# Optimization experiments

Measured on AMD Instinct MI355X. Metric: run time of the kernel, lower is better.

The kernel has to match this reference:

```python
import jax, jax.numpy as jnp
import numpy as np

B, T, I = 4096, 256, 8
H1, H2 = 100, 50


def _init(key, shape, fan):
    # PyTorch LSTM/Linear default: U(-1/sqrt(fan), 1/sqrt(fan))
    bound = 1.0 / np.sqrt(fan)
    return jax.random.uniform(key, shape, jnp.float32, -bound, bound)


def setup_inputs() -> dict:
    key = jax.random.key(0)
    ks = jax.random.split(key, 12)
    x = jax.random.normal(ks[0], (B, T, I), jnp.float32)
    return {
        "x": x,
        "W_ih1": _init(ks[1], (4 * H1, I), H1),
        "W_hh1": _init(ks[2], (4 * H1, H1), H1),
        "b_ih1": _init(ks[3], (4 * H1,), H1),
        "b_hh1": _init(ks[4], (4 * H1,), H1),
        "W_ih2": _init(ks[5], (4 * H2, H1), H2),
        "W_hh2": _init(ks[6], (4 * H2, H2), H2),
        "b_ih2": _init(ks[7], (4 * H2,), H2),
        "b_hh2": _init(ks[8], (4 * H2,), H2),
        "Wd": _init(ks[9], (1, H2), H2),
        "bd": _init(ks[10], (1,), H2),
    }


def _lstm_layer(x, W_ih, W_hh, b_ih, b_hh, H, return_seq):
    # x: [B, T, F]. PyTorch gate order: i, f, g, o. Zero initial state.
    Bn = x.shape[0]
    xg = jnp.einsum("btf,gf->btg", x, W_ih) + b_ih + b_hh  # [B, T, 4H]

    def step(carry, xg_t):
        h, c = carry
        g = xg_t + h @ W_hh.T  # [B, 4H]
        i, f, gg, o = jnp.split(g, 4, axis=-1)
        c = jax.nn.sigmoid(f) * c + jax.nn.sigmoid(i) * jnp.tanh(gg)
        h = jax.nn.sigmoid(o) * jnp.tanh(c)
        return (h, c), (h if return_seq else 0.0)

    init = (jnp.zeros((Bn, H), x.dtype), jnp.zeros((Bn, H), x.dtype))
    (h_last, _), hs = jax.lax.scan(step, init, jnp.swapaxes(xg, 0, 1))
    if return_seq:
        return jnp.swapaxes(hs, 0, 1)  # [B, T, H]
    return h_last  # [B, H]


def reference(x, W_ih1, W_hh1, b_ih1, b_hh1, W_ih2, W_hh2, b_ih2, b_hh2, Wd, bd):
    out1 = _lstm_layer(x, W_ih1, W_hh1, b_ih1, b_hh1, H1, return_seq=True)
    h2 = _lstm_layer(out1, W_ih2, W_hh2, b_ih2, b_hh2, H2, return_seq=False)
    # dropout(p=0.2) is identity in eval mode
    return h2 @ Wd.T + bd  # [B, 1]
```

## Files before the change

### kernel.cpp

```cpp
#include <hip/hip_runtime.h>
#include <math.h>

#define TT 256
#define H1 100
#define H2 50
#define NT 512
#define NBLK 256
#define ROWS 16

typedef __attribute__((ext_vector_type(8))) short bf16x8;
typedef __attribute__((ext_vector_type(4))) float f32x4;

__device__ __forceinline__ float sigf(float x) {
    return __builtin_amdgcn_rcpf(1.0f + __expf(-x));
}
__device__ __forceinline__ float tanhfast(float x) {
    return 1.0f - 2.0f * __builtin_amdgcn_rcpf(1.0f + __expf(2.0f * x));
}
__device__ __forceinline__ short f2bf(float f) {
    union { float f; unsigned u; } v; v.f = f;
    unsigned r = v.u + 0x7FFFu + ((v.u >> 16) & 1u);
    return (short)(r >> 16);
}

__device__ __forceinline__ int off_frag(int K, int R) {
    return (K >> 5) * 1024 + ((K >> 3) & 3) * 256 + R * 16 + (K & 7) * 2;
}

#define MFMA(w, b, c) __builtin_amdgcn_mfma_f32_16x16x32_bf16(w, b, c, 0, 0, 0)

__device__ __forceinline__ float cellup(const f32x4& a, float& cst) {
    const float is = sigf(a[0]), fs = sigf(a[1]);
    const float gt = tanhfast(a[2]), os = sigf(a[3]);
    const float c = fs * cst + is * gt;
    cst = c;
    return os * tanhfast(c);
}

__device__ __forceinline__ void load_w1(bf16x8* dst, int T, int r, int q,
                                        const float* W_hh1, const float* W_ih1) {
    const int jp = T * 16 + r, g = jp & 3, uu = jp >> 2;
#pragma unroll
    for (int c = 0; c < 4; ++c) {
        bf16x8 w;
#pragma unroll
        for (int i = 0; i < 8; ++i) {
            const int k = c * 32 + q * 8 + i;
            float f = 0.f;
            if (k < H1) f = W_hh1[(g * H1 + uu) * H1 + k];
            else if (k < H1 + 8) f = W_ih1[(g * H1 + uu) * 8 + (k - H1)];
            w[i] = f2bf(f);
        }
        dst[c] = w;
    }
}
__device__ __forceinline__ void load_w2(bf16x8* dst, int t2, int r, int q,
                                        const float* W_ih2, const float* W_hh2) {
    const int jp = t2 * 16 + r, g = jp & 3, uu = jp >> 2;
    const bool ok = uu < H2;
#pragma unroll
    for (int c = 0; c < 6; ++c) {
        bf16x8 w;
#pragma unroll
        for (int i = 0; i < 8; ++i) {
            float f = 0.f;
            if (ok) {
                if (c < 4) {
                    const int k = c * 32 + q * 8 + i;
                    if (k < H1) f = W_ih2[(g * H2 + uu) * H1 + k];
                } else {
                    const int k2 = (c - 4) * 32 + q * 8 + i;
                    if (k2 < H2) f = W_hh2[(g * H2 + uu) * H2 + k2];
                }
            }
            w[i] = f2bf(f);
        }
        dst[c] = w;
    }
}

__global__ __launch_bounds__(NT, 2) void lstm_ws3(
    const float* __restrict__ x,
    const float* __restrict__ W_ih1, const float* __restrict__ W_hh1,
    const float* __restrict__ b_ih1, const float* __restrict__ b_hh1,
    const float* __restrict__ W_ih2, const float* __restrict__ W_hh2,
    const float* __restrict__ b_ih2, const float* __restrict__ b_hh2,
    const float* __restrict__ Wd, const float* __restrict__ bd,
    float* __restrict__ out)
{
    __shared__ __align__(16) short xb[TT * ROWS * 8];
    __shared__ __align__(16) short A1h[2 * 4 * 64 * 8];
    __shared__ __align__(16) short h2b[2 * 2 * 64 * 8];
    __shared__ float hscr[ROWS * 52];

    const int tid = threadIdx.x;
    const int lane = tid & 63;
    const int wv = tid >> 6;
    const int r = lane & 15;
    const int q = lane >> 4;
    const int row0 = blockIdx.x * ROWS;

    char* const a1b = (char*)A1h;
    char* const h2bb = (char*)h2b;

    {
        const float* xg = x + (size_t)row0 * (TT * 8);
        for (int it = 0; it < 16; ++it) {
            const int f = (it * NT + tid) * 4;
            const float4 v = *(const float4*)(xg + f);
            const int rr = f >> 11, rem = f & 2047, t = rem >> 3, k = rem & 7;
            uint2 pk;
            pk.x = (unsigned short)f2bf(v.x) | ((unsigned)(unsigned short)f2bf(v.y) << 16);
            pk.y = (unsigned short)f2bf(v.z) | ((unsigned)(unsigned short)f2bf(v.w) << 16);
            *(uint2*)((char*)xb + t * 256 + rr * 16 + k * 2) = pk;
        }
    }
    for (int i = tid; i < 2 * 4 * 64 * 8; i += NT) A1h[i] = 0;
    for (int i = tid; i < 2 * 2 * 64 * 8; i += NT) h2b[i] = 0;

    bf16x8 wfA0[4], wfA1[4], wfA2[4], wfB[6], wfC[6];
    f32x4 bv0, bv1, bv2, bv3 = {0.f, 0.f, 0.f, 0.f}, bv4;
    int wof0, wof1, wof2, wof3 = 0, wof4;
    int hso3 = 0, hso4;
    bool ok3 = false;

    load_w1(wfA0, wv + 0, r, q, W_hh1, W_ih1);
    load_w1(wfA1, wv + 8, r, q, W_hh1, W_ih1);
    load_w1(wfA2, wv + 16, r, q, W_hh1, W_ih1);
    {
        const int u0 = (wv + 0) * 4 + q, u1 = (wv + 8) * 4 + q, u2_ = (wv + 16) * 4 + q;
#pragma unroll
        for (int g = 0; g < 4; ++g) {
            bv0[g] = b_ih1[g * H1 + u0] + b_hh1[g * H1 + u0];
            bv1[g] = b_ih1[g * H1 + u1] + b_hh1[g * H1 + u1];
            bv2[g] = b_ih1[g * H1 + u2_] + b_hh1[g * H1 + u2_];
        }
        wof0 = off_frag(u0, r); wof1 = off_frag(u1, r); wof2 = off_frag(u2_, r);
    }
    if (wv == 0) {
        load_w1(wfB, 24, r, q, W_hh1, W_ih1);
        wfB[4] = (bf16x8){0,0,0,0,0,0,0,0};
        wfB[5] = (bf16x8){0,0,0,0,0,0,0,0};
        const int u = 96 + q;
#pragma unroll
        for (int g = 0; g < 4; ++g) bv3[g] = b_ih1[g * H1 + u] + b_hh1[g * H1 + u];
        wof3 = off_frag(u, r);
        ok3 = true;
    } else if (wv <= 5) {
        load_w2(wfB, wv + 7, r, q, W_ih2, W_hh2);
        const int u2 = (wv + 7) * 4 + q;
        ok3 = (u2 < H2);
#pragma unroll
        for (int g = 0; g < 4; ++g)
            bv3[g] = ok3 ? (b_ih2[g * H2 + u2] + b_hh2[g * H2 + u2]) : 0.f;
        wof3 = off_frag(u2 & 63, r);
        hso3 = r * 52 + u2;
    } else {
#pragma unroll
        for (int c = 0; c < 6; ++c) wfB[c] = (bf16x8){0,0,0,0,0,0,0,0};
    }
    {
        load_w2(wfC, wv, r, q, W_ih2, W_hh2);
        const int u2 = wv * 4 + q;
#pragma unroll
        for (int g = 0; g < 4; ++g) bv4[g] = b_ih2[g * H2 + u2] + b_hh2[g * H2 + u2];
        wof4 = off_frag(u2, r);
        hso4 = r * 52 + u2;
    }

    float cst0 = 0.f, cst1 = 0.f, cst2 = 0.f, cst3 = 0.f, cst4 = 0.f;

    const bool wstage = ((tid >> 4) == 28);
    const int st = tid & 15;

    __syncthreads();
    if (tid < ROWS) {
        bf16x8 v = *(const bf16x8*)((const char*)xb + tid * 16);
        uint2 lo = ((const uint2*)&v)[0], hi = ((const uint2*)&v)[1];
        char* dst = a1b + 3 * 1024 + tid * 16;
        *(uint2*)(dst + 8) = lo;
        *(uint2*)(dst + 256) = hi;
    }
    __syncthreads();

    for (int s = 0; s < TT; ++s) {
        const int cur = s & 1;
        char* a1r = a1b + (cur << 12);
        char* h2r = h2bb + (cur << 11);
        char* a1w = a1b + ((cur ^ 1) << 12);
        char* h2w = h2bb + ((cur ^ 1) << 11);

        const bf16x8 bA0 = *(const bf16x8*)(a1r + 0 * 1024 + lane * 16);
        const bf16x8 bA1 = *(const bf16x8*)(a1r + 1 * 1024 + lane * 16);
        const bf16x8 bA2 = *(const bf16x8*)(a1r + 2 * 1024 + lane * 16);
        const bf16x8 bA3 = *(const bf16x8*)(a1r + 3 * 1024 + lane * 16);
        const bf16x8 bH0 = *(const bf16x8*)(h2r + 0 * 1024 + lane * 16);
        const bf16x8 bH1 = *(const bf16x8*)(h2r + 1 * 1024 + lane * 16);

        if (wstage && s + 1 < TT) {
            bf16x8 v = *(const bf16x8*)((const char*)xb + (s + 1) * 256 + st * 16);
            uint2 lo = ((const uint2*)&v)[0], hi = ((const uint2*)&v)[1];
            char* dst = a1w + 3 * 1024 + st * 16;
            *(uint2*)(dst + 8) = lo;
            *(uint2*)(dst + 256) = hi;
        }

        f32x4 a0 = MFMA(wfA0[0], bA0, bv0);
        f32x4 a1 = MFMA(wfA1[0], bA0, bv1);
        f32x4 a2 = MFMA(wfA2[0], bA0, bv2);
        f32x4 a3 = MFMA(wfB[0], bA0, bv3);
        f32x4 a4 = MFMA(wfC[0], bA0, bv4);
        a0 = MFMA(wfA0[1], bA1, a0);
        a1 = MFMA(wfA1[1], bA1, a1);
        a2 = MFMA(wfA2[1], bA1, a2);
        a3 = MFMA(wfB[1], bA1, a3);
        a4 = MFMA(wfC[1], bA1, a4);
        a0 = MFMA(wfA0[2], bA2, a0);
        a1 = MFMA(wfA1[2], bA2, a1);
        a2 = MFMA(wfA2[2], bA2, a2);
        a3 = MFMA(wfB[2], bA2, a3);
        a4 = MFMA(wfC[2], bA2, a4);
        a0 = MFMA(wfA0[3], bA3, a0);
        a1 = MFMA(wfA1[3], bA3, a1);
        a2 = MFMA(wfA2[3], bA3, a2);
        a3 = MFMA(wfB[3], bA3, a3);
        a4 = MFMA(wfC[3], bA3, a4);
        a3 = MFMA(wfB[4], bH0, a3);
        a4 = MFMA(wfC[4], bH0, a4);
        a3 = MFMA(wfB[5], bH1, a3);
        a4 = MFMA(wfC[5], bH1, a4);

        const float h0 = cellup(a0, cst0);
        const float h1v = cellup(a1, cst1);
        const float h2v = cellup(a2, cst2);
        *(short*)(a1w + wof0) = f2bf(h0);
        *(short*)(a1w + wof1) = f2bf(h1v);
        *(short*)(a1w + wof2) = f2bf(h2v);

        if (s > 0) {
            const float h4v = cellup(a4, cst4);
            *(short*)(h2w + wof4) = f2bf(h4v);
        }
        if (wv == 0 || (s > 0 && wv <= 5)) {
            const float h3v = cellup(a3, cst3);
            char* d3 = (wv == 0) ? a1w : h2w;
            if (ok3) *(short*)(d3 + wof3) = f2bf(h3v);
        }
        __syncthreads();
    }

    {
        char* a1r = a1b;
        char* h2r = h2bb;
        const bf16x8 bA0 = *(const bf16x8*)(a1r + 0 * 1024 + lane * 16);
        const bf16x8 bA1 = *(const bf16x8*)(a1r + 1 * 1024 + lane * 16);
        const bf16x8 bA2 = *(const bf16x8*)(a1r + 2 * 1024 + lane * 16);
        const bf16x8 bA3 = *(const bf16x8*)(a1r + 3 * 1024 + lane * 16);
        const bf16x8 bH0 = *(const bf16x8*)(h2r + 0 * 1024 + lane * 16);
        const bf16x8 bH1 = *(const bf16x8*)(h2r + 1 * 1024 + lane * 16);

        f32x4 a3 = MFMA(wfB[0], bA0, bv3);
        f32x4 a4 = MFMA(wfC[0], bA0, bv4);
        a3 = MFMA(wfB[1], bA1, a3);
        a4 = MFMA(wfC[1], bA1, a4);
        a3 = MFMA(wfB[2], bA2, a3);
        a4 = MFMA(wfC[2], bA2, a4);
        a3 = MFMA(wfB[3], bA3, a3);
        a4 = MFMA(wfC[3], bA3, a4);
        a3 = MFMA(wfB[4], bH0, a3);
        a4 = MFMA(wfC[4], bH0, a4);
        a3 = MFMA(wfB[5], bH1, a3);
        a4 = MFMA(wfC[5], bH1, a4);

        if (wv >= 1 && wv <= 5) {
            const float h3v = cellup(a3, cst3);
            if (ok3) hscr[hso3] = h3v;
        }
        {
            const float h4v = cellup(a4, cst4);
            hscr[hso4] = h4v;
        }
        __syncthreads();
    }

    if (tid < ROWS) {
        float acc = bd[0];
#pragma unroll 2
        for (int u = 0; u < H2; ++u) acc = fmaf(hscr[tid * 52 + u], Wd[u], acc);
        out[row0 + tid] = acc;
    }
}

extern "C" void kernel_launch(void* const* d_in, const int* in_sizes, int n_in,
                              void* d_out, int out_size, void* d_ws, size_t ws_size,
                              hipStream_t stream) {
    const float* x     = (const float*)d_in[0];
    const float* W_ih1 = (const float*)d_in[1];
    const float* W_hh1 = (const float*)d_in[2];
    const float* b_ih1 = (const float*)d_in[3];
    const float* b_hh1 = (const float*)d_in[4];
    const float* W_ih2 = (const float*)d_in[5];
    const float* W_hh2 = (const float*)d_in[6];
    const float* b_ih2 = (const float*)d_in[7];
    const float* b_hh2 = (const float*)d_in[8];
    const float* Wd    = (const float*)d_in[9];
    const float* bd    = (const float*)d_in[10];
    float* out = (float*)d_out;

    hipLaunchKernelGGL(lstm_ws3, dim3(NBLK), dim3(NT), 0, stream,
                       x, W_ih1, W_hh1, b_ih1, b_hh1,
                       W_ih2, W_hh2, b_ih2, b_hh2, Wd, bd, out);
}
```

Baseline: 380.0 us.

## Double waves per block to spread LSTM gate tiles across 16 wavefronts

The block grows from 8 to 16 wavefronts, and each wave now owns at most three gate tiles instead of five. The 25 layer-1 tiles and 13 layer-2 tiles are reassigned: waves 0-8 take two layer-1 tiles, waves 9-15 take one layer-1 and one layer-2 tile, and waves 0-5 take an extra layer-2 tile. The aim is to shorten the serial MFMA and cell-update chain per wave on every timestep. In exchange, each barrier now synchronises more waves, and occupancy drops from 2 blocks per CU to 1 with a 1024-thread block.

Result: faster. 367.8 us (-3.2%).

```diff
diff --git a/kernel.cpp b/kernel.cpp
--- a/kernel.cpp
+++ b/kernel.cpp
@@ -4,7 +4,7 @@
 #define TT 256
 #define H1 100
 #define H2 50
-#define NT 512
+#define NT 1024
 #define NBLK 256
 #define ROWS 16
 
@@ -54,32 +54,38 @@
         dst[c] = w;
     }
 }
-__device__ __forceinline__ void load_w2(bf16x8* dst, int t2, int r, int q,
+__device__ __forceinline__ void load_w2(bf16x8* dstA, bf16x8* dstH, int t2,
+                                        int r, int q,
                                         const float* W_ih2, const float* W_hh2) {
     const int jp = t2 * 16 + r, g = jp & 3, uu = jp >> 2;
     const bool ok = uu < H2;
 #pragma unroll
-    for (int c = 0; c < 6; ++c) {
+    for (int c = 0; c < 4; ++c) {
         bf16x8 w;
 #pragma unroll
         for (int i = 0; i < 8; ++i) {
+            const int k = c * 32 + q * 8 + i;
             float f = 0.f;
-            if (ok) {
-                if (c < 4) {
-                    const int k = c * 32 + q * 8 + i;
-                    if (k < H1) f = W_ih2[(g * H2 + uu) * H1 + k];
-                } else {
-                    const int k2 = (c - 4) * 32 + q * 8 + i;
-                    if (k2 < H2) f = W_hh2[(g * H2 + uu) * H2 + k2];
-                }
-            }
+            if (ok && k < H1) f = W_ih2[(g * H2 + uu) * H1 + k];
             w[i] = f2bf(f);
         }
-        dst[c] = w;
-    }
-}
-
-__global__ __launch_bounds__(NT, 2) void lstm_ws3(
+        dstA[c] = w;
+    }
+#pragma unroll
+    for (int c = 0; c < 2; ++c) {
+        bf16x8 w;
+#pragma unroll
+        for (int i = 0; i < 8; ++i) {
+            const int k2 = c * 32 + q * 8 + i;
+            float f = 0.f;
+            if (ok && k2 < H2) f = W_hh2[(g * H2 + uu) * H2 + k2];
+            w[i] = f2bf(f);
+        }
+        dstH[c] = w;
+    }
+}
+
+__global__ __launch_bounds__(NT) void lstm_ws5(
     const float* __restrict__ x,
     const float* __restrict__ W_ih1, const float* __restrict__ W_hh1,
     const float* __restrict__ b_ih1, const float* __restrict__ b_hh1,
@@ -105,7 +111,8 @@
 
     {
         const float* xg = x + (size_t)row0 * (TT * 8);
-        for (int it = 0; it < 16; ++it) {
+#pragma unroll
+        for (int it = 0; it < 8; ++it) {
             const int f = (it * NT + tid) * 4;
             const float4 v = *(const float4*)(xg + f);
             const int rr = f >> 11, rem = f & 2047, t = rem >> 3, k = rem & 7;
@@ -117,60 +124,57 @@
     }
     for (int i = tid; i < 2 * 4 * 64 * 8; i += NT) A1h[i] = 0;
     for (int i = tid; i < 2 * 2 * 64 * 8; i += NT) h2b[i] = 0;
-
-    bf16x8 wfA0[4], wfA1[4], wfA2[4], wfB[6], wfC[6];
-    f32x4 bv0, bv1, bv2, bv3 = {0.f, 0.f, 0.f, 0.f}, bv4;
-    int wof0, wof1, wof2, wof3 = 0, wof4;
-    int hso3 = 0, hso4;
-    bool ok3 = false;
-
-    load_w1(wfA0, wv + 0, r, q, W_hh1, W_ih1);
-    load_w1(wfA1, wv + 8, r, q, W_hh1, W_ih1);
-    load_w1(wfA2, wv + 16, r, q, W_hh1, W_ih1);
+    if (tid < ROWS * 52) hscr[tid] = 0.f;
+
+    const bool s1isL1 = (wv <= 8);
+    const bool hasS2 = (wv <= 5);
+
+    bf16x8 wf0[4], wf1[4], wf2[4], wH[2];
+    const bf16x8 zf = (bf16x8){0, 0, 0, 0, 0, 0, 0, 0};
+#pragma unroll
+    for (int c = 0; c < 4; ++c) wf2[c] = zf;
+    wH[0] = zf; wH[1] = zf;
+
+    f32x4 bv0, bv1, bv2 = {0.f, 0.f, 0.f, 0.f};
+    int wof0, wof1, wof2 = 0;
+    int hso1 = 0, hso2 = 0;
+    bool ok2 = false;
+
+    load_w1(wf0, wv, r, q, W_hh1, W_ih1);
     {
-        const int u0 = (wv + 0) * 4 + q, u1 = (wv + 8) * 4 + q, u2_ = (wv + 16) * 4 + q;
-#pragma unroll
-        for (int g = 0; g < 4; ++g) {
-            bv0[g] = b_ih1[g * H1 + u0] + b_hh1[g * H1 + u0];
-            bv1[g] = b_ih1[g * H1 + u1] + b_hh1[g * H1 + u1];
-            bv2[g] = b_ih1[g * H1 + u2_] + b_hh1[g * H1 + u2_];
-        }
-        wof0 = off_frag(u0, r); wof1 = off_frag(u1, r); wof2 = off_frag(u2_, r);
-    }
-    if (wv == 0) {
-        load_w1(wfB, 24, r, q, W_hh1, W_ih1);
-        wfB[4] = (bf16x8){0,0,0,0,0,0,0,0};
-        wfB[5] = (bf16x8){0,0,0,0,0,0,0,0};
-        const int u = 96 + q;
-#pragma unroll
-        for (int g = 0; g < 4; ++g) bv3[g] = b_ih1[g * H1 + u] + b_hh1[g * H1 + u];
-        wof3 = off_frag(u, r);
-        ok3 = true;
-    } else if (wv <= 5) {
-        load_w2(wfB, wv + 7, r, q, W_ih2, W_hh2);
-        const int u2 = (wv + 7) * 4 + q;
-        ok3 = (u2 < H2);
+        const int u0 = wv * 4 + q;
+#pragma unroll
+        for (int g = 0; g < 4; ++g) bv0[g] = b_ih1[g * H1 + u0] + b_hh1[g * H1 + u0];
+        wof0 = off_frag(u0, r);
+    }
+    if (s1isL1) {
+        load_w1(wf1, 16 + wv, r, q, W_hh1, W_ih1);
+        const int u1 = (16 + wv) * 4 + q;
+#pragma unroll
+        for (int g = 0; g < 4; ++g) bv1[g] = b_ih1[g * H1 + u1] + b_hh1[g * H1 + u1];
+        wof1 = off_frag(u1, r);
+    } else {
+        load_w2(wf1, wH, wv - 9, r, q, W_ih2, W_hh2);
+        const int u21 = (wv - 9) * 4 + q;
+#pragma unroll
+        for (int g = 0; g < 4; ++g) bv1[g] = b_ih2[g * H2 + u21] + b_hh2[g * H2 + u21];
+        wof1 = off_frag(u21, r);
+        hso1 = r * 52 + u21;
+    }
+    if (hasS2) {
+        load_w2(wf2, wH, 7 + wv, r, q, W_ih2, W_hh2);
+        const int u22 = (7 + wv) * 4 + q;
+        ok2 = (u22 < H2);
 #pragma unroll
         for (int g = 0; g < 4; ++g)
-            bv3[g] = ok3 ? (b_ih2[g * H2 + u2] + b_hh2[g * H2 + u2]) : 0.f;
-        wof3 = off_frag(u2 & 63, r);
-        hso3 = r * 52 + u2;
-    } else {
-#pragma unroll
-        for (int c = 0; c < 6; ++c) wfB[c] = (bf16x8){0,0,0,0,0,0,0,0};
-    }
-    {
-        load_w2(wfC, wv, r, q, W_ih2, W_hh2);
-        const int u2 = wv * 4 + q;
-#pragma unroll
-        for (int g = 0; g < 4; ++g) bv4[g] = b_ih2[g * H2 + u2] + b_hh2[g * H2 + u2];
-        wof4 = off_frag(u2, r);
-        hso4 = r * 52 + u2;
-    }
-
-    float cst0 = 0.f, cst1 = 0.f, cst2 = 0.f, cst3 = 0.f, cst4 = 0.f;
-
-    const bool wstage = ((tid >> 4) == 28);
+            bv2[g] = ok2 ? (b_ih2[g * H2 + u22] + b_hh2[g * H2 + u22]) : 0.f;
+        wof2 = off_frag(u22 & 63, r);
+        hso2 = r * 52 + u22;
+    }
+
+    float cst0 = 0.f, cst1 = 0.f, cst2 = 0.f;
+
+    const bool wstage = ((tid >> 4) == 60);
     const int st = tid & 15;
 
     __syncthreads();
@@ -205,46 +209,41 @@
             *(uint2*)(dst + 256) = hi;
         }
 
-        f32x4 a0 = MFMA(wfA0[0], bA0, bv0);
-        f32x4 a1 = MFMA(wfA1[0], bA0, bv1);
-        f32x4 a2 = MFMA(wfA2[0], bA0, bv2);
-        f32x4 a3 = MFMA(wfB[0], bA0, bv3);
-        f32x4 a4 = MFMA(wfC[0], bA0, bv4);
-        a0 = MFMA(wfA0[1], bA1, a0);
-        a1 = MFMA(wfA1[1], bA1, a1);
-        a2 = MFMA(wfA2[1], bA1, a2);
-        a3 = MFMA(wfB[1], bA1, a3);
-        a4 = MFMA(wfC[1], bA1, a4);
-        a0 = MFMA(wfA0[2], bA2, a0);
-        a1 = MFMA(wfA1[2], bA2, a1);
-        a2 = MFMA(wfA2[2], bA2, a2);
-        a3 = MFMA(wfB[2], bA2, a3);
-        a4 = MFMA(wfC[2], bA2, a4);
-        a0 = MFMA(wfA0[3], bA3, a0);
-        a1 = MFMA(wfA1[3], bA3, a1);
-        a2 = MFMA(wfA2[3], bA3, a2);
-        a3 = MFMA(wfB[3], bA3, a3);
-        a4 = MFMA(wfC[3], bA3, a4);
-        a3 = MFMA(wfB[4], bH0, a3);
-        a4 = MFMA(wfC[4], bH0, a4);
-        a3 = MFMA(wfB[5], bH1, a3);
-        a4 = MFMA(wfC[5], bH1, a4);
+        f32x4 a0 = MFMA(wf0[0], bA0, bv0);
+        f32x4 a1 = MFMA(wf1[0], bA0, bv1);
+        a0 = MFMA(wf0[1], bA1, a0);
+        a1 = MFMA(wf1[1], bA1, a1);
+        a0 = MFMA(wf0[2], bA2, a0);
+        a1 = MFMA(wf1[2], bA2, a1);
+        a0 = MFMA(wf0[3], bA3, a0);
+        a1 = MFMA(wf1[3], bA3, a1);
+        if (!s1isL1) {
+            a1 = MFMA(wH[0], bH0, a1);
+            a1 = MFMA(wH[1], bH1, a1);
+        }
+        f32x4 a2 = bv2;
+        if (hasS2) {
+            a2 = MFMA(wf2[0], bA0, a2);
+            a2 = MFMA(wf2[1], bA1, a2);
+            a2 = MFMA(wf2[2], bA2, a2);
+            a2 = MFMA(wf2[3], bA3, a2);
+            a2 = MFMA(wH[0], bH0, a2);
+            a2 = MFMA(wH[1], bH1, a2);
+        }
 
         const float h0 = cellup(a0, cst0);
-        const float h1v = cellup(a1, cst1);
-        const float h2v = cellup(a2, cst2);
         *(short*)(a1w + wof0) = f2bf(h0);
-        *(short*)(a1w + wof1) = f2bf(h1v);
-        *(short*)(a1w + wof2) = f2bf(h2v);
-
-        if (s > 0) {
-            const float h4v = cellup(a4, cst4);
-            *(short*)(h2w + wof4) = f2bf(h4v);
-        }
-        if (wv == 0 || (s > 0 && wv <= 5)) {
-            const float h3v = cellup(a3, cst3);
-            char* d3 = (wv == 0) ? a1w : h2w;
-            if (ok3) *(short*)(d3 + wof3) = f2bf(h3v);
+
+        if (s1isL1) {
+            const float h1v = cellup(a1, cst1);
+            *(short*)(a1w + wof1) = f2bf(h1v);
+        } else if (s > 0) {
+            const float h1v = cellup(a1, cst1);
+            *(short*)(h2w + wof1) = f2bf(h1v);
+        }
+        if (hasS2 && s > 0) {
+            const float h2v = cellup(a2, cst2);
+            if (ok2) *(short*)(h2w + wof2) = f2bf(h2v);
         }
         __syncthreads();
     }
@@ -252,33 +251,35 @@
     {
         char* a1r = a1b;
         char* h2r = h2bb;
-        const bf16x8 bA0 = *(const bf16x8*)(a1r + 0 * 1024 + lane * 16);
-        const bf16x8 bA1 = *(const bf16x8*)(a1r + 1 * 1024 + lane * 16);
-        const bf16x8 bA2 = *(const bf16x8*)(a1r + 2 * 1024 + lane * 16);
-        const bf16x8 bA3 = *(const bf16x8*)(a1r + 3 * 1024 + lane * 16);
-        const bf16x8 bH0 = *(const bf16x8*)(h2r + 0 * 1024 + lane * 16);
-        const bf16x8 bH1 = *(const bf16x8*)(h2r + 1 * 1024 + lane * 16);
-
-        f32x4 a3 = MFMA(wfB[0], bA0, bv3);
-        f32x4 a4 = MFMA(wfC[0], bA0, bv4);
-        a3 = MFMA(wfB[1], bA1, a3);
-        a4 = MFMA(wfC[1], bA1, a4);
-        a3 = MFMA(wfB[2], bA2, a3);
-        a4 = MFMA(wfC[2], bA2, a4);
-        a3 = MFMA(wfB[3], bA3, a3);
-        a4 = MFMA(wfC[3], bA3, a4);
-        a3 = MFMA(wfB[4], bH0, a3);
-        a4 = MFMA(wfC[4], bH0, a4);
-        a3 = MFMA(wfB[5], bH1, a3);
-        a4 = MFMA(wfC[5], bH1, a4);
-
-        if (wv >= 1 && wv <= 5) {
-            const float h3v = cellup(a3, cst3);
-            if (ok3) hscr[hso3] = h3v;
-        }
-        {
-            const float h4v = cellup(a4, cst4);
-            hscr[hso4] = h4v;
+        if (!s1isL1 || hasS2) {
+            const bf16x8 bA0 = *(const bf16x8*)(a1r + 0 * 1024 + lane * 16);
+            const bf16x8 bA1 = *(const bf16x8*)(a1r + 1 * 1024 + lane * 16);
+            const bf16x8 bA2 = *(const bf16x8*)(a1r + 2 * 1024 + lane * 16);
+            const bf16x8 bA3 = *(const bf16x8*)(a1r + 3 * 1024 + lane * 16);
+            const bf16x8 bH0 = *(const bf16x8*)(h2r + 0 * 1024 + lane * 16);
+            const bf16x8 bH1 = *(const bf16x8*)(h2r + 1 * 1024 + lane * 16);
+
+            if (!s1isL1) {
+                f32x4 a1 = MFMA(wf1[0], bA0, bv1);
+                a1 = MFMA(wf1[1], bA1, a1);
+                a1 = MFMA(wf1[2], bA2, a1);
+                a1 = MFMA(wf1[3], bA3, a1);
+                a1 = MFMA(wH[0], bH0, a1);
+                a1 = MFMA(wH[1], bH1, a1);
+                const float h1v = cellup(a1, cst1);
+                hscr[hso1] = h1v;
+            }
+            if (hasS2) {
+                f32x4 a2 = bv2;
+                a2 = MFMA(wf2[0], bA0, a2);
+                a2 = MFMA(wf2[1], bA1, a2);
+                a2 = MFMA(wf2[2], bA2, a2);
+                a2 = MFMA(wf2[3], bA3, a2);
+                a2 = MFMA(wH[0], bH0, a2);
+                a2 = MFMA(wH[1], bH1, a2);
+                const float h2v = cellup(a2, cst2);
+                if (ok2) hscr[hso2] = h2v;
+            }
         }
         __syncthreads();
     }
@@ -307,7 +308,7 @@
     const float* bd    = (const float*)d_in[10];
     float* out = (float*)d_out;
 
-    hipLaunchKernelGGL(lstm_ws3, dim3(NBLK), dim3(NT), 0, stream,
+    hipLaunchKernelGGL(lstm_ws5, dim3(NBLK), dim3(NT), 0, stream,
                        x, W_ih1, W_hh1, b_ih1, b_hh1,
                        W_ih2, W_hh2, b_ih2, b_hh2, Wd, bd, out);
 }
```
